# Optimization experiments

Hardware: AMD Instinct MI355X
Metric: run time of the kernel (lower is better)

Reference implementation:

```python
import jax, jax.numpy as jnp
import numpy as np

N = 50000      # nodes (square sparse matrix shape[0] == shape[1])
NNZ = 1600000  # edges = N * avg_degree(32)
B = 2          # batch of feature matrices
D = 128        # feature dim


def setup_inputs() -> dict:
    key = jax.random.key(0)
    k1, k2, k3 = jax.random.split(key, 3)
    indices = jax.random.randint(k1, (2, NNZ), 0, N, dtype=jnp.int32)  # [2, nnz] COO (row, col)
    values = jax.random.uniform(k2, (NNZ,), dtype=jnp.float32)          # [nnz] edge values
    b = jax.random.normal(k3, (B, N, D), dtype=jnp.float32)             # [B, N, D] dense features
    return {"indices": indices, "values": values, "n": N, "b": b}


def reference(indices, values, n, b):
    # out = sparse_coo(indices, values, (n, n)) @ b, batched over b's leading dim.
    # True SpMM: gather source-node features, scale by edge value, segment-sum
    # into destination rows. Duplicate indices are summed (same as coalesce()).
    rows, cols = indices[0], indices[1]
    def spmm_one(feat):  # feat: [N, D]
        gathered = values[:, None] * feat[cols]              # [nnz, D]
        return jax.ops.segment_sum(gathered, rows, num_segments=n)  # [N, D]
    return jax.vmap(spmm_one)(b)  # [B, N, D]
```

## Files before the change

kernel.cpp:

```cpp
#include <hip/hip_runtime.h>


#define FEAT_D 128
#define BATCH 2
#define RB_SHIFT 8
#define NB_MAX 256
#define BCAP 10240
#define PART_E 8192
#define PART_T 512
#define PACK_BLOCKS 1024

typedef int   iv4 __attribute__((ext_vector_type(4)));
typedef float fv4 __attribute__((ext_vector_type(4)));
typedef unsigned uv2 __attribute__((ext_vector_type(2)));

__device__ inline unsigned short f32_to_bf16_rne(float f) {
  unsigned u = __float_as_uint(f);
  unsigned r = u + 0x7fffu + ((u >> 16) & 1u);
  return (unsigned short)(r >> 16);
}

__device__ inline uv2 tbl_load(const unsigned short* pbase, unsigned p) {
  return *reinterpret_cast<const uv2*>(pbase + ((size_t)(p & 0xffffu) << 8));
}
__device__ inline void fma_edge(fv4& acc, unsigned p, uv2 w) {
  const float v = __uint_as_float(p & 0xffff0000u);
  acc.x += v * __uint_as_float(w.x << 16);
  acc.y += v * __uint_as_float(w.x & 0xffff0000u);
  acc.z += v * __uint_as_float(w.y << 16);
  acc.w += v * __uint_as_float(w.y & 0xffff0000u);
}

__global__ void __launch_bounds__(NB_MAX) init_fixed_kernel(
    int* __restrict__ bbase, int* __restrict__ gcur, int nb) {
  const int t = threadIdx.x;
  if (t < nb) {
    bbase[t] = t * BCAP;
    gcur[t] = t * BCAP;
  }
}

__global__ void __launch_bounds__(256) hist_bucket_kernel(
    const int* __restrict__ rows, int nnz, int* __restrict__ bcnt) {
  __shared__ int h[256];
  h[threadIdx.x] = 0;
  __syncthreads();
  const int n4 = nnz >> 2;
  for (int i = blockIdx.x * blockDim.x + threadIdx.x; i < n4;
       i += gridDim.x * blockDim.x) {
    const iv4 r4 = *(reinterpret_cast<const iv4*>(rows) + i);
    atomicAdd(&h[r4.x >> RB_SHIFT], 1);
    atomicAdd(&h[r4.y >> RB_SHIFT], 1);
    atomicAdd(&h[r4.z >> RB_SHIFT], 1);
    atomicAdd(&h[r4.w >> RB_SHIFT], 1);
  }
  if (blockIdx.x == 0 && threadIdx.x < (nnz & 3))
    atomicAdd(&h[rows[(n4 << 2) + threadIdx.x] >> RB_SHIFT], 1);
  __syncthreads();
  if (h[threadIdx.x]) atomicAdd(&bcnt[threadIdx.x], h[threadIdx.x]);
}

__global__ void __launch_bounds__(256) scan_buckets_kernel(
    const int* __restrict__ bcnt, int nb,
    int* __restrict__ bbase, int* __restrict__ gcur) {
  __shared__ int sc[256];
  const int tid = threadIdx.x;
  const int v = (tid < nb) ? bcnt[tid] : 0;
  sc[tid] = v;
  __syncthreads();
  for (int off = 1; off < 256; off <<= 1) {
    int t = (tid >= off) ? sc[tid - off] : 0;
    __syncthreads();
    sc[tid] += t;
    __syncthreads();
  }
  const int excl = sc[tid] - v;
  if (tid < nb) {
    bbase[tid] = excl;
    gcur[tid] = excl;
  }
}

__device__ inline void partition_body(
    const int* __restrict__ rows, const int* __restrict__ cols,
    const float* __restrict__ vals, int nnz, int nb,
    int* __restrict__ gcur,
    unsigned* __restrict__ cvb_key, unsigned short* __restrict__ cvb_val,
    int blk, int* hist, int* excl, int* cur, int* gdst,
    unsigned* stage_key, unsigned short* stage_val, unsigned char* slotb) {
  const int tid = threadIdx.x;
  const int base = blk * PART_E;
  const int cnt = min(PART_E, nnz - base);

  if (tid < 256) hist[tid] = 0;
  __syncthreads();

  for (int k = tid; k < cnt; k += PART_T)
    atomicAdd(&hist[rows[base + k] >> RB_SHIFT], 1);
  __syncthreads();

  if (tid < 256) excl[tid] = hist[tid];
  __syncthreads();
  for (int off = 1; off < 256; off <<= 1) {
    int v = 0;
    if (tid < 256 && tid >= off) v = excl[tid - off];
    __syncthreads();
    if (tid < 256) excl[tid] += v;
    __syncthreads();
  }
  if (tid < 256) {
    const int e = excl[tid] - hist[tid];
    excl[tid] = e;
    cur[tid] = e;
    int gd = 0;
    if (tid < nb && hist[tid] > 0) {
      const int gb = atomicAdd(&gcur[tid], hist[tid]);
      gd = gb - e;
    }
    gdst[tid] = gd;
  }
  __syncthreads();

  for (int k = tid; k < cnt; k += PART_T) {
    const int e = base + k;
    const int r = rows[e];
    const int c = __builtin_nontemporal_load(&cols[e]);
    const float v = __builtin_nontemporal_load(&vals[e]);
    const int b = r >> RB_SHIFT;
    const int pos = atomicAdd(&cur[b], 1);
    stage_key[pos] = (unsigned)(((r & 255) << 16) | c);
    stage_val[pos] = f32_to_bf16_rne(v);
    slotb[pos] = (unsigned char)b;
  }
  __syncthreads();

  for (int i = tid; i < cnt; i += PART_T) {
    const int b = slotb[i];
    const int idx = gdst[b] + i;
    cvb_key[idx] = stage_key[i];
    cvb_val[idx] = stage_val[i];
  }
}

__global__ void __launch_bounds__(PART_T) partition_kernel(
    const int* __restrict__ rows, const int* __restrict__ cols,
    const float* __restrict__ vals, int nnz, int nb,
    int* __restrict__ gcur,
    unsigned* __restrict__ cvb_key, unsigned short* __restrict__ cvb_val) {
  __shared__ int hist[256];
  __shared__ int excl[256];
  __shared__ int cur[256];
  __shared__ int gdst[256];
  __shared__ unsigned stage_key[PART_E];
  __shared__ unsigned short stage_val[PART_E];
  __shared__ unsigned char slotb[PART_E];
  partition_body(rows, cols, vals, nnz, nb, gcur, cvb_key, cvb_val, blockIdx.x,
                 hist, excl, cur, gdst, stage_key, stage_val, slotb);
}

__global__ void __launch_bounds__(PART_T) partpack_kernel(
    const int* __restrict__ rows, const int* __restrict__ cols,
    const float* __restrict__ vals, int nnz, int nb,
    int* __restrict__ gcur,
    unsigned* __restrict__ cvb_key, unsigned short* __restrict__ cvb_val,
    const float* __restrict__ feat, unsigned short* __restrict__ packed,
    int n, int part_blocks) {
  __shared__ int hist[256];
  __shared__ int excl[256];
  __shared__ int cur[256];
  __shared__ int gdst[256];
  __shared__ unsigned stage_key[PART_E];
  __shared__ unsigned short stage_val[PART_E];
  __shared__ unsigned char slotb[PART_E];

  if ((int)blockIdx.x < part_blocks) {
    partition_body(rows, cols, vals, nnz, nb, gcur, cvb_key, cvb_val, blockIdx.x,
                   hist, excl, cur, gdst, stage_key, stage_val, slotb);
  } else {
    const int pb = blockIdx.x - part_blocks;
    const int npb = gridDim.x - part_blocks;
    const int total = n * (BATCH * FEAT_D / 4);
    for (int q = pb * PART_T + threadIdx.x; q < total; q += npb * PART_T) {
      const int r = q >> 6;
      const int rem = q & 63;
      const int b = rem >> 5;
      const int d4 = rem & 31;
      const fv4 x = __builtin_nontemporal_load(reinterpret_cast<const fv4*>(
          feat + ((size_t)b * n + r) * FEAT_D + (size_t)d4 * 4));
      unsigned a0 = (unsigned)f32_to_bf16_rne(x.x) | ((unsigned)f32_to_bf16_rne(x.y) << 16);
      unsigned a1 = (unsigned)f32_to_bf16_rne(x.z) | ((unsigned)f32_to_bf16_rne(x.w) << 16);
      uv2 o; o.x = a0; o.y = a1;
      *reinterpret_cast<uv2*>(packed + (size_t)q * 4) = o;
    }
  }
}

__global__ void __launch_bounds__(256) bucket_sort_kernel(
    const unsigned* __restrict__ cvb_key, const unsigned short* __restrict__ cvb_val,
    const int* __restrict__ bbase, const int* __restrict__ gcur,
    int* __restrict__ offsets, int* __restrict__ rowend,
    unsigned* __restrict__ cv, int n) {
  __shared__ int h[256];
  __shared__ int sc[256];
  __shared__ int cur[256];
  const int tid = threadIdx.x;
  const int b = blockIdx.x;
  const int start = bbase[b];
  const int end = gcur[b];

  h[tid] = 0;
  __syncthreads();
  for (int i = start + tid; i < end; i += 256)
    atomicAdd(&h[cvb_key[i] >> 16], 1);
  __syncthreads();
  sc[tid] = h[tid];
  __syncthreads();
  for (int off = 1; off < 256; off <<= 1) {
    int t = (tid >= off) ? sc[tid - off] : 0;
    __syncthreads();
    sc[tid] += t;
    __syncthreads();
  }
  const int excl = sc[tid] - h[tid];
  const int row = (b << RB_SHIFT) + tid;
  if (row < n) {
    offsets[row] = start + excl;
    rowend[row] = start + excl + h[tid];
  }
  cur[tid] = start + excl;
  __syncthreads();
  for (int i = start + tid; i < end; i += 256) {
    const unsigned key = cvb_key[i];
    const unsigned val = (unsigned)cvb_val[i];
    const int pos = atomicAdd(&cur[key >> 16], 1);
    cv[pos] = (val << 16) | (key & 0xffffu);
  }
}

__global__ void __launch_bounds__(256) pack_kernel(
    const float* __restrict__ feat, unsigned short* __restrict__ packed, int n) {
  const int q = blockIdx.x * blockDim.x + threadIdx.x;
  const int total = n * (BATCH * FEAT_D / 4);
  if (q >= total) return;
  const int r = q >> 6;
  const int rem = q & 63;
  const int b = rem >> 5;
  const int d4 = rem & 31;
  const fv4 x = __builtin_nontemporal_load(reinterpret_cast<const fv4*>(
      feat + ((size_t)b * n + r) * FEAT_D + (size_t)d4 * 4));
  unsigned a0 = (unsigned)f32_to_bf16_rne(x.x) | ((unsigned)f32_to_bf16_rne(x.y) << 16);
  unsigned a1 = (unsigned)f32_to_bf16_rne(x.z) | ((unsigned)f32_to_bf16_rne(x.w) << 16);
  uv2 o; o.x = a0; o.y = a1;
  *reinterpret_cast<uv2*>(packed + (size_t)q * 4) = o;
}

__global__ void __launch_bounds__(256) spmm_seg_bf16_kernel(
    const int* __restrict__ offsets, const int* __restrict__ rowend,
    const unsigned* __restrict__ cv,
    const unsigned short* __restrict__ packed,
    float* __restrict__ out, int n) {
  const int wid = (int)((blockIdx.x * (unsigned)blockDim.x + threadIdx.x) >> 6);
  if (wid >= n) return;
  const int lane = threadIdx.x & 63;

  int start = __builtin_amdgcn_readfirstlane(offsets[wid]);
  int end = __builtin_amdgcn_readfirstlane(rowend[wid]);

  const unsigned short* pbase = packed + (size_t)lane * 4;

  fv4 acc; acc.x = 0.f; acc.y = 0.f; acc.z = 0.f; acc.w = 0.f;
  int i = start;
  for (; i + 8 <= end; i += 8) {
    const unsigned p0 = __builtin_nontemporal_load(&cv[i + 0]);
    const unsigned p1 = __builtin_nontemporal_load(&cv[i + 1]);
    const unsigned p2 = __builtin_nontemporal_load(&cv[i + 2]);
    const unsigned p3 = __builtin_nontemporal_load(&cv[i + 3]);
    const unsigned p4 = __builtin_nontemporal_load(&cv[i + 4]);
    const unsigned p5 = __builtin_nontemporal_load(&cv[i + 5]);
    const unsigned p6 = __builtin_nontemporal_load(&cv[i + 6]);
    const unsigned p7 = __builtin_nontemporal_load(&cv[i + 7]);
    const uv2 w0 = tbl_load(pbase, p0);
    const uv2 w1 = tbl_load(pbase, p1);
    const uv2 w2 = tbl_load(pbase, p2);
    const uv2 w3 = tbl_load(pbase, p3);
    const uv2 w4 = tbl_load(pbase, p4);
    const uv2 w5 = tbl_load(pbase, p5);
    const uv2 w6 = tbl_load(pbase, p6);
    const uv2 w7 = tbl_load(pbase, p7);
    fma_edge(acc, p0, w0);
    fma_edge(acc, p1, w1);
    fma_edge(acc, p2, w2);
    fma_edge(acc, p3, w3);
    fma_edge(acc, p4, w4);
    fma_edge(acc, p5, w5);
    fma_edge(acc, p6, w6);
    fma_edge(acc, p7, w7);
  }
  for (; i < end; ++i) {
    const unsigned p = __builtin_nontemporal_load(&cv[i]);
    fma_edge(acc, p, tbl_load(pbase, p));
  }

  const int half = lane >> 5;
  const int l32 = lane & 31;
  const size_t bs = (size_t)n * FEAT_D;
  float* dst = out + (size_t)half * bs + (size_t)wid * FEAT_D + (size_t)l32 * 4;
  __builtin_nontemporal_store(acc, reinterpret_cast<fv4*>(dst));
}

__global__ void __launch_bounds__(256) spmm_atomic_kernel(
    const int* __restrict__ indices, const float* __restrict__ values,
    const float* __restrict__ feat, float* __restrict__ out, int nnz, int n) {
  const long long gid = (long long)blockIdx.x * blockDim.x + threadIdx.x;
  const int lane = (int)(gid & 31);
  const long long e = gid >> 5;
  if (e >= nnz) return;
  const int r = indices[e];
  const int c = indices[(long long)nnz + e];
  const float v = values[e];
  const size_t bs = (size_t)n * FEAT_D;
  for (int b = 0; b < BATCH; ++b) {
    const float4 a = *(reinterpret_cast<const float4*>(feat + b * bs + (size_t)c * FEAT_D) + lane);
    float* dst = out + b * bs + (size_t)r * FEAT_D + (size_t)lane * 4;
    atomicAdd(dst + 0, v * a.x);
    atomicAdd(dst + 1, v * a.y);
    atomicAdd(dst + 2, v * a.z);
    atomicAdd(dst + 3, v * a.w);
  }
}

static inline size_t align256(size_t x) { return (x + 255) & ~(size_t)255; }

extern "C" void kernel_launch(void* const* d_in, const int* in_sizes, int n_in,
                              void* d_out, int out_size, void* d_ws, size_t ws_size,
                              hipStream_t stream) {
  const int* indices = (const int*)d_in[0];
  const float* values = (const float*)d_in[1];
  const float* feat = (const float*)d_in[3];
  float* out = (float*)d_out;

  const int nnz = in_sizes[1];
  const int n = out_size / (BATCH * FEAT_D);
  const int nb = (n + 255) >> RB_SHIFT;

  const int* rows = indices;
  const int* cols = indices + nnz;

  size_t off_offsets = 0;
  size_t off_rowend = off_offsets + (size_t)n * 4;
  size_t off_bcnt = off_rowend + (size_t)n * 4;
  size_t off_bbase = off_bcnt + (size_t)NB_MAX * 4;
  size_t off_gcur = off_bbase + (size_t)NB_MAX * 4;
  size_t off_cv = align256(off_gcur + (size_t)NB_MAX * 4);

  const size_t packed_bytes = (size_t)n * BATCH * FEAT_D * 2;
  const size_t entA = (size_t)nb * BCAP;
  const size_t entC = (size_t)nnz;

  const size_t offA_key = align256(off_cv + entA * 4);
  const size_t offA_val = align256(offA_key + entA * 4);
  const size_t offA_packed = align256(offA_val + entA * 2);
  const size_t needA = offA_packed + packed_bytes;
  const size_t offC_key = align256(off_cv + entC * 4);
  const size_t offC_val = align256(offC_key + entC * 4);
  const size_t offC_packed = align256(offC_val + entC * 2);
  const size_t needC = offC_packed + packed_bytes;

  const int avg = nnz / (nb > 0 ? nb : 1);
  const bool cap_ok = (avg + avg / 8 + 256) < BCAP;
  const bool shape_ok = (n <= (NB_MAX << RB_SHIFT)) && (nb <= NB_MAX) && (n <= 65536);

  if (!shape_ok || ws_size < needC) {
    hipMemsetAsync(d_out, 0, (size_t)out_size * sizeof(float), stream);
    const long long total_threads = (long long)nnz * 32;
    const unsigned grid = (unsigned)((total_threads + 255) / 256);
    spmm_atomic_kernel<<<grid, 256, 0, stream>>>(indices, values, feat, out, nnz, n);
    return;
  }

  char* ws = (char*)d_ws;
  int* offsets = (int*)(ws + off_offsets);
  int* rowend = (int*)(ws + off_rowend);
  int* bcnt = (int*)(ws + off_bcnt);
  int* bbase = (int*)(ws + off_bbase);
  int* gcur = (int*)(ws + off_gcur);
  unsigned* cv = (unsigned*)(ws + off_cv);

  const int part_blocks = (nnz + PART_E - 1) / PART_E;
  const int pack_total = n * (BATCH * FEAT_D / 4);
  const unsigned seg_grid = (unsigned)(((long long)n * 64 + 255) / 256);

  if (cap_ok && ws_size >= needA) {
    unsigned* cvb_key = (unsigned*)(ws + offA_key);
    unsigned short* cvb_val = (unsigned short*)(ws + offA_val);
    unsigned short* packed = (unsigned short*)(ws + offA_packed);
    init_fixed_kernel<<<1, NB_MAX, 0, stream>>>(bbase, gcur, nb);
    partpack_kernel<<<part_blocks + PACK_BLOCKS, PART_T, 0, stream>>>(
        rows, cols, values, nnz, nb, gcur, cvb_key, cvb_val, feat, packed, n, part_blocks);
    bucket_sort_kernel<<<nb, 256, 0, stream>>>(cvb_key, cvb_val, bbase, gcur,
                                               offsets, rowend, cv, n);
    spmm_seg_bf16_kernel<<<seg_grid, 256, 0, stream>>>(offsets, rowend, cv, packed, out, n);
  } else {
    unsigned* cvb_key = (unsigned*)(ws + offC_key);
    unsigned short* cvb_val = (unsigned short*)(ws + offC_val);
    unsigned short* packed = (unsigned short*)(ws + offC_packed);
    hipMemsetAsync(bcnt, 0, (size_t)NB_MAX * 4, stream);
    hist_bucket_kernel<<<512, 256, 0, stream>>>(rows, nnz, bcnt);
    scan_buckets_kernel<<<1, 256, 0, stream>>>(bcnt, nb, bbase, gcur);
    partition_kernel<<<part_blocks, PART_T, 0, stream>>>(rows, cols, values, nnz, nb,
                                                         gcur, cvb_key, cvb_val);
    bucket_sort_kernel<<<nb, 256, 0, stream>>>(cvb_key, cvb_val, bbase, gcur,
                                               offsets, rowend, cv, n);
    pack_kernel<<<(pack_total + 255) / 256, 256, 0, stream>>>(feat, packed, n);
    spmm_seg_bf16_kernel<<<seg_grid, 256, 0, stream>>>(offsets, rowend, cv, packed, out, n);
  }
}
```

Measured before the change: 165.9 us.

## Split SpMM by batch and divide each row's edges between wave halves

The segmented SpMM kernel now runs once per batch element. Each 64-lane wave splits a row's edges between its two 32-lane halves, each half handling alternate edges for the same batch, and the halves are combined with a cross-half shuffle before a single store. The intent is to halve per-row serial edge latency and shrink each kernel's gather footprint to one batch slice. In exchange it adds a second launch, reads the index stream twice, and adds a shuffle reduction.

```diff
diff --git a/kernel.cpp b/kernel.cpp
--- a/kernel.cpp
+++ b/kernel.cpp
@@ -254,58 +254,55 @@
   *reinterpret_cast<uv2*>(packed + (size_t)q * 4) = o;
 }
 
-__global__ void __launch_bounds__(256) spmm_seg_bf16_kernel(
+__global__ void __launch_bounds__(256) spmm_seg_split_kernel(
     const int* __restrict__ offsets, const int* __restrict__ rowend,
     const unsigned* __restrict__ cv,
     const unsigned short* __restrict__ packed,
-    float* __restrict__ out, int n) {
+    float* __restrict__ out, int n, int batch) {
   const int wid = (int)((blockIdx.x * (unsigned)blockDim.x + threadIdx.x) >> 6);
   if (wid >= n) return;
   const int lane = threadIdx.x & 63;
+  const int half = lane >> 5;
+  const int l32 = lane & 31;
 
   int start = __builtin_amdgcn_readfirstlane(offsets[wid]);
   int end = __builtin_amdgcn_readfirstlane(rowend[wid]);
 
-  const unsigned short* pbase = packed + (size_t)lane * 4;
+  const unsigned short* pbase = packed + (size_t)batch * FEAT_D + (size_t)l32 * 4;
 
   fv4 acc; acc.x = 0.f; acc.y = 0.f; acc.z = 0.f; acc.w = 0.f;
   int i = start;
   for (; i + 8 <= end; i += 8) {
-    const unsigned p0 = __builtin_nontemporal_load(&cv[i + 0]);
-    const unsigned p1 = __builtin_nontemporal_load(&cv[i + 1]);
-    const unsigned p2 = __builtin_nontemporal_load(&cv[i + 2]);
-    const unsigned p3 = __builtin_nontemporal_load(&cv[i + 3]);
-    const unsigned p4 = __builtin_nontemporal_load(&cv[i + 4]);
-    const unsigned p5 = __builtin_nontemporal_load(&cv[i + 5]);
-    const unsigned p6 = __builtin_nontemporal_load(&cv[i + 6]);
-    const unsigned p7 = __builtin_nontemporal_load(&cv[i + 7]);
+    const unsigned p0 = __builtin_nontemporal_load(&cv[i + 0 + half]);
+    const unsigned p1 = __builtin_nontemporal_load(&cv[i + 2 + half]);
+    const unsigned p2 = __builtin_nontemporal_load(&cv[i + 4 + half]);
+    const unsigned p3 = __builtin_nontemporal_load(&cv[i + 6 + half]);
     const uv2 w0 = tbl_load(pbase, p0);
     const uv2 w1 = tbl_load(pbase, p1);
     const uv2 w2 = tbl_load(pbase, p2);
     const uv2 w3 = tbl_load(pbase, p3);
-    const uv2 w4 = tbl_load(pbase, p4);
-    const uv2 w5 = tbl_load(pbase, p5);
-    const uv2 w6 = tbl_load(pbase, p6);
-    const uv2 w7 = tbl_load(pbase, p7);
     fma_edge(acc, p0, w0);
     fma_edge(acc, p1, w1);
     fma_edge(acc, p2, w2);
     fma_edge(acc, p3, w3);
-    fma_edge(acc, p4, w4);
-    fma_edge(acc, p5, w5);
-    fma_edge(acc, p6, w6);
-    fma_edge(acc, p7, w7);
-  }
-  for (; i < end; ++i) {
-    const unsigned p = __builtin_nontemporal_load(&cv[i]);
+  }
+  for (; i < end; i += 2) {
+    const int idx = i + half;
+    unsigned p = 0;
+    if (idx < end) p = __builtin_nontemporal_load(&cv[idx]);
     fma_edge(acc, p, tbl_load(pbase, p));
   }
 
-  const int half = lane >> 5;
-  const int l32 = lane & 31;
-  const size_t bs = (size_t)n * FEAT_D;
-  float* dst = out + (size_t)half * bs + (size_t)wid * FEAT_D + (size_t)l32 * 4;
-  __builtin_nontemporal_store(acc, reinterpret_cast<fv4*>(dst));
+  acc.x += __shfl_xor(acc.x, 32);
+  acc.y += __shfl_xor(acc.y, 32);
+  acc.z += __shfl_xor(acc.z, 32);
+  acc.w += __shfl_xor(acc.w, 32);
+
+  if (half == 0) {
+    const size_t bs = (size_t)n * FEAT_D;
+    float* dst = out + (size_t)batch * bs + (size_t)wid * FEAT_D + (size_t)l32 * 4;
+    __builtin_nontemporal_store(acc, reinterpret_cast<fv4*>(dst));
+  }
 }
 
 __global__ void __launch_bounds__(256) spmm_atomic_kernel(
@@ -399,7 +396,8 @@
         rows, cols, values, nnz, nb, gcur, cvb_key, cvb_val, feat, packed, n, part_blocks);
     bucket_sort_kernel<<<nb, 256, 0, stream>>>(cvb_key, cvb_val, bbase, gcur,
                                                offsets, rowend, cv, n);
-    spmm_seg_bf16_kernel<<<seg_grid, 256, 0, stream>>>(offsets, rowend, cv, packed, out, n);
+    spmm_seg_split_kernel<<<seg_grid, 256, 0, stream>>>(offsets, rowend, cv, packed, out, n, 0);
+    spmm_seg_split_kernel<<<seg_grid, 256, 0, stream>>>(offsets, rowend, cv, packed, out, n, 1);
   } else {
     unsigned* cvb_key = (unsigned*)(ws + offC_key);
     unsigned short* cvb_val = (unsigned short*)(ws + offC_val);
@@ -412,6 +410,7 @@
     bucket_sort_kernel<<<nb, 256, 0, stream>>>(cvb_key, cvb_val, bbase, gcur,
                                                offsets, rowend, cv, n);
     pack_kernel<<<(pack_total + 255) / 256, 256, 0, stream>>>(feat, packed, n);
-    spmm_seg_bf16_kernel<<<seg_grid, 256, 0, stream>>>(offsets, rowend, cv, packed, out, n);
-  }
-}
+    spmm_seg_split_kernel<<<seg_grid, 256, 0, stream>>>(offsets, rowend, cv, packed, out, n, 0);
+    spmm_seg_split_kernel<<<seg_grid, 256, 0, stream>>>(offsets, rowend, cv, packed, out, n, 1);
+  }
+}
```

Result: slower. 173.0 us (+4.3%).
